# Kernel tuning notes

Measured on AMD Instinct MI355X. Metric: run time of the kernel, lower is better.

The kernel has to match this reference:

```python
import jax, jax.numpy as jnp
import numpy as np

HID, E, S, L_CAP, EPS = 768, 1536, 128, 512, 1e-5


def _rope_seq(x):
    """RoPE along axis 1. x: [b, n, 2, s]."""
    n, s = x.shape[1], x.shape[-1]
    half = s // 2
    inv_freq = jnp.power(10000.0, -jnp.arange(half, dtype=x.dtype) / half)  # [half]
    sinusoid = jnp.arange(n, dtype=x.dtype)[:, None, None] * inv_freq       # [n,1,half]
    sin, cos = jnp.sin(sinusoid), jnp.cos(sinusoid)
    x1, x2 = jnp.split(x, 2, axis=-1)
    return jnp.concatenate([x1 * cos - x2 * sin, x2 * cos + x1 * sin], axis=-1)


def setup_inputs() -> dict:
    key = jax.random.key(0)
    ks = jax.random.split(key, 6)
    B, L = 32, 512
    return {
        "x": jax.random.normal(ks[0], (B, L, HID), dtype=jnp.float32),
        "ln_gamma": jnp.ones((HID,), jnp.float32),
        "ln_beta": jnp.zeros((HID,), jnp.float32),
        "uv_W": jax.random.normal(ks[1], (HID, 2 * E + S), jnp.float32) * 0.02,
        "uv_b": jnp.zeros((2 * E + S,), jnp.float32),
        "gamma_qk": jax.random.normal(ks[2], (2, S), jnp.float32) * 0.02,
        "beta_qk": jnp.zeros((2, S), jnp.float32),
        "w_rel": jax.random.normal(ks[3], (2 * L_CAP - 1,), jnp.float32) * 0.02,
        "o_W": jax.random.normal(ks[4], (E, HID), jnp.float32) * 0.02,
        "o_b": jnp.zeros((HID,), jnp.float32),
    }


def reference(x, ln_gamma, ln_beta, uv_W, uv_b, gamma_qk, beta_qk, w_rel, o_W, o_b):
    L = x.shape[1]
    shortcut = x
    # LayerNorm
    mu = jnp.mean(x, axis=-1, keepdims=True)
    var = jnp.mean(jnp.square(x - mu), axis=-1, keepdims=True)
    xn = (x - mu) * jax.lax.rsqrt(var + EPS) * ln_gamma + ln_beta
    # uv projection + silu, split into u, v, base
    uv = jax.nn.silu(xn @ uv_W + uv_b)                       # [b, n, 2e+s]
    u, v, base = jnp.split(uv, [E, 2 * E], axis=-1)          # [b,n,e], [b,n,e], [b,n,s]
    # per-head affine then RoPE -> q, k
    base = base[..., None, :] * gamma_qk + beta_qk           # [b, n, 2, s]
    base = _rope_seq(base)
    q, k = base[..., 0, :], base[..., 1, :]
    # relu^2 attention kernel with Toeplitz relative position bias
    qk = jnp.einsum('bnd,bmd->bnm', q, k)
    idx = jnp.arange(L)
    bias = w_rel[idx[None, :] - idx[:, None] + L - 1]        # bias[i,j] = w[j-i+L-1]
    kernel = jnp.square(jax.nn.relu(qk / L + bias))
    # gated value aggregation + output projection + residual
    out = u * jnp.einsum('bnm,bme->bne', kernel, v)
    out = out @ o_W + o_b
    return out + shortcut
```

## Files before the change

kernel.cpp:

```cpp
#include <hip/hip_runtime.h>
#include <hip/hip_bf16.h>
#include <math.h>

typedef __bf16 bf16x8 __attribute__((ext_vector_type(8)));
typedef float f32x4 __attribute__((ext_vector_type(4)));
typedef unsigned short u16x4 __attribute__((ext_vector_type(4)));

#define AS1P const __attribute__((address_space(1))) void*
#define AS3P __attribute__((address_space(3))) void*

__device__ __forceinline__ float b2f(unsigned short h) {
    unsigned int u = ((unsigned int)h) << 16;
    return __builtin_bit_cast(float, u);
}
__device__ __forceinline__ unsigned short f2b(float f) {
    unsigned int u = __builtin_bit_cast(unsigned int, f);
    u += 0x7FFFu + ((u >> 16) & 1u);
    return (unsigned short)(u >> 16);
}
__device__ __forceinline__ float silu(float c) {
    return c * __builtin_amdgcn_rcpf(1.0f + __expf(-c));
}

__global__ __launch_bounds__(256) void k_convT(const float* __restrict__ src,
                                               unsigned short* __restrict__ dst,
                                               int R, int C) {
    __shared__ float tile[32][33];
    int tx = threadIdx.x, ty = threadIdx.y;
    int r0 = blockIdx.y << 5, c0 = blockIdx.x << 5;
#pragma unroll
    for (int i = 0; i < 4; ++i)
        tile[ty + 8 * i][tx] = src[(long long)(r0 + ty + 8 * i) * C + c0 + tx];
    __syncthreads();
#pragma unroll
    for (int i = 0; i < 4; ++i)
        dst[(long long)(c0 + ty + 8 * i) * R + r0 + tx] = f2b(tile[tx][ty + 8 * i]);
}

__global__ __launch_bounds__(256) void k_ln(const float* __restrict__ x,
                                            const float* __restrict__ g,
                                            const float* __restrict__ b,
                                            unsigned short* __restrict__ xn) {
    int row = blockIdx.x;
    int t = threadIdx.x;
    const float* xr = x + (long long)row * 768;
    float v0 = xr[t], v1 = xr[t + 256], v2 = xr[t + 512];
    float s = v0 + v1 + v2;
    float q = v0 * v0 + v1 * v1 + v2 * v2;
#pragma unroll
    for (int off = 32; off > 0; off >>= 1) {
        s += __shfl_xor(s, off);
        q += __shfl_xor(q, off);
    }
    __shared__ float ss[4], sq[4];
    int w = t >> 6;
    if ((t & 63) == 0) { ss[w] = s; sq[w] = q; }
    __syncthreads();
    float S_ = ss[0] + ss[1] + ss[2] + ss[3];
    float Q_ = sq[0] + sq[1] + sq[2] + sq[3];
    float mu = S_ * (1.0f / 768.0f);
    float var = Q_ * (1.0f / 768.0f) - mu * mu;
    float rs = rsqrtf(var + 1e-5f);
    unsigned short* xo = xn + (long long)row * 768;
    xo[t]       = f2b((v0 - mu) * rs * g[t]       + b[t]);
    xo[t + 256] = f2b((v1 - mu) * rs * g[t + 256] + b[t + 256]);
    xo[t + 512] = f2b((v2 - mu) * rs * g[t + 512] + b[t + 512]);
}

__global__ __launch_bounds__(128) void k_rope(const unsigned short* __restrict__ bS,
                                              const float* __restrict__ gqk,
                                              const float* __restrict__ bqk,
                                              unsigned short* __restrict__ q,
                                              unsigned short* __restrict__ k) {
    int row = blockIdx.x;
    int l = row & 511;
    int s = threadIdx.x;
    int j = s & 63;
    int partner = s ^ 64;
    float b0 = b2f(bS[(long long)row * 128 + s]);
    float bp = b2f(bS[(long long)row * 128 + partner]);
    float invf = __expf((float)j * -0.14391156831f);
    float th = (float)l * invf;
    float sn, cs;
    __sincosf(th, &sn, &cs);
    float sign = (s < 64) ? -1.0f : 1.0f;
    float preq  = b0 * gqk[s]           + bqk[s];
    float preqp = bp * gqk[partner]     + bqk[partner];
    q[(long long)row * 128 + s] = f2b(preq * cs + sign * preqp * sn);
    float prek  = b0 * gqk[128 + s]       + bqk[128 + s];
    float prekp = bp * gqk[128 + partner] + bqk[128 + partner];
    k[(long long)row * 128 + s] = f2b(prek * cs + sign * prekp * sn);
}

__global__ __launch_bounds__(256) void k_qk(const unsigned short* __restrict__ A,
                                            const unsigned short* __restrict__ B,
                                            const float* __restrict__ wrel,
                                            unsigned short* __restrict__ P) {
    __shared__ __align__(16) unsigned short As[128 * 64];
    __shared__ __align__(16) unsigned short Bs[128 * 64];
    int t = threadIdx.x;
    int w = t >> 6, lane = t & 63;
    int wr = w >> 1, wc = w & 1;
    int bx = blockIdx.x, by = blockIdx.y, bz = blockIdx.z;
    const unsigned short* Ab = A + (long long)bz * 512 * 128 + (long long)by * 128 * 128;
    const unsigned short* Bb = B + (long long)bz * 512 * 128 + (long long)bx * 128 * 128;

    f32x4 acc[4][4];
#pragma unroll
    for (int m = 0; m < 4; ++m)
#pragma unroll
        for (int n = 0; n < 4; ++n) acc[m][n] = (f32x4){0.f, 0.f, 0.f, 0.f};

    int rowA = (w << 3) + (lane >> 3);
    int colA = (lane & 7) << 3;

    for (int k0 = 0; k0 < 128; k0 += 64) {
#pragma unroll
        for (int i = 0; i < 4; ++i) {
            int r = (i << 5) + rowA;
            __builtin_amdgcn_global_load_lds(
                (AS1P)(Ab + (long long)r * 128 + k0 + colA),
                (AS3P)(&As[(i << 11) + (w << 9)]), 16, 0, 0);
            __builtin_amdgcn_global_load_lds(
                (AS1P)(Bb + (long long)r * 128 + k0 + colA),
                (AS3P)(&Bs[(i << 11) + (w << 9)]), 16, 0, 0);
        }
        __syncthreads();
#pragma unroll
        for (int ks = 0; ks < 2; ++ks) {
            bf16x8 af[4], bfr[4];
#pragma unroll
            for (int m = 0; m < 4; ++m)
                af[m] = *(const bf16x8*)&As[((wr << 6) + (m << 4) + (lane & 15)) * 64 +
                                            (ks << 5) + ((lane >> 4) << 3)];
#pragma unroll
            for (int n = 0; n < 4; ++n)
                bfr[n] = *(const bf16x8*)&Bs[((wc << 6) + (n << 4) + (lane & 15)) * 64 +
                                             (ks << 5) + ((lane >> 4) << 3)];
#pragma unroll
            for (int m = 0; m < 4; ++m)
#pragma unroll
                for (int n = 0; n < 4; ++n)
                    acc[m][n] = __builtin_amdgcn_mfma_f32_16x16x32_bf16(bfr[n], af[m],
                                                                        acc[m][n], 0, 0, 0);
        }
        __syncthreads();
    }

    int c15 = lane & 15, qq = lane >> 4;
    int rowb = (by << 7) + (wr << 6) + c15;
    int colb = (bx << 7) + (wc << 6) + (qq << 2);
#pragma unroll
    for (int m = 0; m < 4; ++m) {
#pragma unroll
        for (int n = 0; n < 4; ++n) {
            int grow = rowb + (m << 4);
            int gcol = colb + (n << 4);
            f32x4 a = acc[m][n];
            int base = gcol - grow + 511;
            u16x4 o;
#pragma unroll
            for (int i = 0; i < 4; ++i) {
                float val = a[i] * (1.0f / 512.0f) + wrel[base + i];
                val = fmaxf(val, 0.0f);
                o[i] = f2b(val * val);
            }
            *(u16x4*)(P + ((long long)(bz * 512 + grow)) * 512 + gcol) = o;
        }
    }
}

__device__ __forceinline__ bf16x8 ldsread(const unsigned short* p) {
    bf16x8 r;
    unsigned int off =
        (unsigned int)(unsigned long long)(__attribute__((address_space(3))) const void*)p;
    asm volatile("ds_read_b128 %0, %1" : "=v"(r) : "v"(off));
    return r;
}
__device__ __forceinline__ bf16x8 frag32(const unsigned short* tile, int r, int qq) {
    return ldsread(tile + r * 32 + ((qq ^ ((r >> 1) & 3)) << 3));
}
template <int ROWS, int K>
__device__ __forceinline__ void stage_t(const unsigned short* __restrict__ g,
                                        unsigned short* lds, int t) {
#pragma unroll
    for (int i = 0; i < ROWS / 64; ++i) {
        int slot = t + (i << 8);
        int row = slot >> 2;
        int gs = (slot & 3) ^ ((row >> 1) & 3);
        __builtin_amdgcn_global_load_lds(
            (AS1P)(g + (long long)row * K + (gs << 3)),
            (AS3P)(lds + slot * 8), 16, 0, 0);
    }
}

template <bool SWAP, int NT>
__device__ __forceinline__ void ring_kloop(const unsigned short* __restrict__ Ab,
                                           const unsigned short* __restrict__ Bb,
                                           unsigned short* As0, unsigned short* As1,
                                           unsigned short* Bs0, unsigned short* Bs1,
                                           f32x4 (&acc)[8][4], int t, int wc, int c15, int qq) {
    constexpr int K = NT * 32;
    stage_t<128, K>(Ab, As0, t);
    stage_t<256, K>(Bb, Bs0, t);
    stage_t<128, K>(Ab + 32, As1, t);
    stage_t<256, K>(Bb + 32, Bs1, t);
    for (int kt = 0; kt < NT; ++kt) {
        if (kt < NT - 1)
            asm volatile("s_waitcnt vmcnt(6)" ::: "memory");
        else
            asm volatile("s_waitcnt vmcnt(0)" ::: "memory");
        __builtin_amdgcn_s_barrier();
        __builtin_amdgcn_sched_barrier(0);
        const unsigned short* At = (kt & 1) ? As1 : As0;
        const unsigned short* Bt = (kt & 1) ? Bs1 : Bs0;
        bf16x8 af[8], bfr[4];
#pragma unroll
        for (int n = 0; n < 4; ++n) bfr[n] = frag32(Bt, wc * 64 + n * 16 + c15, qq);
#pragma unroll
        for (int m = 0; m < 8; ++m) af[m] = frag32(At, m * 16 + c15, qq);
        asm volatile("s_waitcnt lgkmcnt(0)" ::: "memory");
        __builtin_amdgcn_sched_barrier(0);
        __builtin_amdgcn_s_barrier();
        if (kt + 2 < NT) {
            unsigned short* Asn = (kt & 1) ? As1 : As0;
            unsigned short* Bsn = (kt & 1) ? Bs1 : Bs0;
            stage_t<128, K>(Ab + (long long)(kt + 2) * 32, Asn, t);
            stage_t<256, K>(Bb + (long long)(kt + 2) * 32, Bsn, t);
        }
        __builtin_amdgcn_s_setprio(1);
#pragma unroll
        for (int m = 0; m < 8; ++m)
#pragma unroll
            for (int n = 0; n < 4; ++n) {
                if constexpr (SWAP)
                    acc[m][n] = __builtin_amdgcn_mfma_f32_16x16x32_bf16(bfr[n], af[m],
                                                                        acc[m][n], 0, 0, 0);
                else
                    acc[m][n] = __builtin_amdgcn_mfma_f32_16x16x32_bf16(af[m], bfr[n],
                                                                        acc[m][n], 0, 0, 0);
            }
        __builtin_amdgcn_s_setprio(0);
    }
}

template <int EPI, bool SWZ, int NT>
__global__ __launch_bounds__(256, 2) void k_ring(const unsigned short* __restrict__ A,
                                                 const unsigned short* __restrict__ B,
                                                 long long strideA, long long strideB,
                                                 void* p0, void* p1, void* p2,
                                                 const void* p3) {
    constexpr int K = NT * 32;
    __shared__ __align__(16) unsigned short As[2][128 * 32];
    __shared__ __align__(16) unsigned short Bs[2][256 * 32];
    int t = threadIdx.x;
    int w = t >> 6, lane = t & 63;
    int wc = w, c15 = lane & 15, qq = lane >> 4;
    int bx = blockIdx.x, by = blockIdx.y, bz = blockIdx.z;
    if constexpr (SWZ) {
        int gx = gridDim.x;
        int nb = gx * gridDim.y;
        int bid = by * gx + bx;
        int s = (bid & 7) * (nb >> 3) + (bid >> 3);
        bx = s % gx;
        by = s / gx;
    }
    const unsigned short* Ab = A + bz * strideA + (long long)by * 128 * K;
    const unsigned short* Bb = B + bz * strideB + (long long)bx * 256 * K;

    f32x4 acc[8][4];
#pragma unroll
    for (int m = 0; m < 8; ++m)
#pragma unroll
        for (int n = 0; n < 4; ++n) acc[m][n] = (f32x4){0.f, 0.f, 0.f, 0.f};

    bool swapped = true;
    if constexpr (EPI == 10) {
        swapped = !(bx >= 6 && bx < 12);
        if (swapped)
            ring_kloop<true, NT>(Ab, Bb, &As[0][0], &As[1][0], &Bs[0][0], &Bs[1][0],
                                 acc, t, wc, c15, qq);
        else
            ring_kloop<false, NT>(Ab, Bb, &As[0][0], &As[1][0], &Bs[0][0], &Bs[1][0],
                                  acc, t, wc, c15, qq);
    } else {
        ring_kloop<true, NT>(Ab, Bb, &As[0][0], &As[1][0], &Bs[0][0], &Bs[1][0],
                             acc, t, wc, c15, qq);
    }

    if constexpr (EPI == 10) {
        if (swapped) {
            int rowb = by * 128 + c15;
            int colb = bx * 256 + wc * 64 + (qq << 2);
#pragma unroll
            for (int m = 0; m < 8; ++m) {
#pragma unroll
                for (int n = 0; n < 4; ++n) {
                    int R = rowb + m * 16;
                    int C = colb + n * 16;
                    f32x4 a = acc[m][n];
                    if (C < 1536) {
                        f32x4 bb = *(const f32x4*)((const float*)p3 + C);
                        u16x4 o;
#pragma unroll
                        for (int i = 0; i < 4; ++i) o[i] = f2b(silu(a[i] + bb[i]));
                        *(u16x4*)((unsigned short*)p0 + (long long)R * 1536 + C) = o;
                    } else if (C < 3200) {
                        f32x4 bb = *(const f32x4*)((const float*)p3 + C);
                        u16x4 o;
#pragma unroll
                        for (int i = 0; i < 4; ++i) o[i] = f2b(silu(a[i] + bb[i]));
                        *(u16x4*)((unsigned short*)p2 + (long long)R * 128 + (C - 3072)) = o;
                    }
                }
            }
        } else {
            int rowb = by * 128 + (qq << 2);
            int colb = bx * 256 + wc * 64 + c15;
#pragma unroll
            for (int m = 0; m < 8; ++m) {
#pragma unroll
                for (int n = 0; n < 4; ++n) {
                    int R = rowb + m * 16;
                    int C = colb + n * 16;
                    float bias = ((const float*)p3)[C];
                    f32x4 a = acc[m][n];
                    u16x4 o;
#pragma unroll
                    for (int i = 0; i < 4; ++i) o[i] = f2b(silu(a[i] + bias));
                    int bb2 = R >> 9, mm = R & 511;
                    *(u16x4*)((unsigned short*)p1 +
                              ((long long)bb2 * 1536 + (C - 1536)) * 512 + mm) = o;
                }
            }
        }
    } else if constexpr (EPI == 2) {
        int rowb = by * 128 + c15;
        int colb = bx * 256 + wc * 64 + (qq << 2);
#pragma unroll
        for (int m = 0; m < 8; ++m) {
#pragma unroll
            for (int n = 0; n < 4; ++n) {
                int R = rowb + m * 16;
                int C = colb + n * 16;
                f32x4 a = acc[m][n];
                long long idx = ((long long)(bz * 512 + R)) * 1536 + C;
                u16x4 uu = *(const u16x4*)((const unsigned short*)p1 + idx);
                u16x4 o;
#pragma unroll
                for (int i = 0; i < 4; ++i) o[i] = f2b(a[i] * b2f(uu[i]));
                *(u16x4*)((unsigned short*)p0 + idx) = o;
            }
        }
    } else {
        int rowb = by * 128 + c15;
        int colb = bx * 256 + wc * 64 + (qq << 2);
#pragma unroll
        for (int m = 0; m < 8; ++m) {
#pragma unroll
            for (int n = 0; n < 4; ++n) {
                int R = rowb + m * 16;
                int C = colb + n * 16;
                f32x4 a = acc[m][n];
                long long idx = (long long)R * 768 + C;
                f32x4 xv = *(const f32x4*)((const float*)p2 + idx);
                f32x4 ob = *(const f32x4*)((const float*)p1 + C);
                f32x4 o;
#pragma unroll
                for (int i = 0; i < 4; ++i) o[i] = a[i] + ob[i] + xv[i];
                *(f32x4*)((float*)p0 + idx) = o;
            }
        }
    }
}

extern "C" void kernel_launch(void* const* d_in, const int* in_sizes, int n_in,
                              void* d_out, int out_size, void* d_ws, size_t ws_size,
                              hipStream_t stream) {
    const float* x     = (const float*)d_in[0];
    const float* ln_g  = (const float*)d_in[1];
    const float* ln_b  = (const float*)d_in[2];
    const float* uv_W  = (const float*)d_in[3];
    const float* uv_b  = (const float*)d_in[4];
    const float* g_qk  = (const float*)d_in[5];
    const float* b_qk  = (const float*)d_in[6];
    const float* w_rel = (const float*)d_in[7];
    const float* o_W   = (const float*)d_in[8];
    const float* o_b   = (const float*)d_in[9];
    float* out = (float*)d_out;

    char* ws = (char*)d_ws;
    size_t off = 0;
    auto alloc = [&](size_t bytes) {
        void* p = ws + off;
        off += (bytes + 255) & ~(size_t)255;
        return p;
    };
    unsigned short* uvWT = (unsigned short*)alloc(3200ll * 768 * 2);
    unsigned short* oWT  = (unsigned short*)alloc(768ll * 1536 * 2);
    unsigned short* xn   = (unsigned short*)alloc(16384ll * 768 * 2);
    unsigned short* u    = (unsigned short*)alloc(16384ll * 1536 * 2);
    unsigned short* vT   = (unsigned short*)alloc(32ll * 1536 * 512 * 2);
    unsigned short* bS   = (unsigned short*)alloc(16384ll * 128 * 2);
    unsigned short* q    = (unsigned short*)alloc(32ll * 512 * 128 * 2);
    unsigned short* k    = (unsigned short*)alloc(32ll * 512 * 128 * 2);
    unsigned short* P     = xn;
    unsigned short* gated = u;

    k_convT<<<dim3(100, 24), dim3(32, 8), 0, stream>>>(uv_W, uvWT, 768, 3200);
    k_convT<<<dim3(24, 48), dim3(32, 8), 0, stream>>>(o_W, oWT, 1536, 768);
    k_ln<<<16384, 256, 0, stream>>>(x, ln_g, ln_b, xn);
    k_ring<10, true, 24><<<dim3(13, 128), 256, 0, stream>>>(
        xn, uvWT, 0, 0, (void*)u, (void*)vT, (void*)bS, (const void*)uv_b);
    k_rope<<<16384, 128, 0, stream>>>(bS, g_qk, b_qk, q, k);
    k_qk<<<dim3(4, 4, 32), 256, 0, stream>>>(q, k, w_rel, P);
    k_ring<2, false, 16><<<dim3(6, 4, 32), 256, 0, stream>>>(
        P, vT, 512ll * 512, 1536ll * 512, (void*)gated, (void*)u, nullptr, nullptr);
    k_ring<3, true, 48><<<dim3(3, 128), 256, 0, stream>>>(
        gated, oWT, 0, 0, (void*)out, (void*)o_b, (void*)x, nullptr);
}
```

Measured before the change: 300.5 us.

## Triple-buffer LDS ring in GEMM k-loop to drop second barrier

The shared-memory staging for the GEMM k-loop grows from two slots to a three-slot ring. The prefetch of tile kt+2 is now issued right after the top-of-iteration barrier, into the slot last read at kt-1. This removes the second barrier per k-step and lets global-to-LDS loads start earlier, overlapping them with the fragment reads and MFMAs. In exchange, LDS use per block rises from 48KB to 72KB, which could limit occupancy under the two-blocks-per-CU launch bound.

```diff
diff --git a/kernel.cpp b/kernel.cpp
--- a/kernel.cpp
+++ b/kernel.cpp
@@ -197,14 +197,15 @@
 template <bool SWAP, int NT>
 __device__ __forceinline__ void ring_kloop(const unsigned short* __restrict__ Ab,
                                            const unsigned short* __restrict__ Bb,
-                                           unsigned short* As0, unsigned short* As1,
-                                           unsigned short* Bs0, unsigned short* Bs1,
+                                           unsigned short* As, unsigned short* Bs,
                                            f32x4 (&acc)[8][4], int t, int wc, int c15, int qq) {
     constexpr int K = NT * 32;
-    stage_t<128, K>(Ab, As0, t);
-    stage_t<256, K>(Bb, Bs0, t);
-    stage_t<128, K>(Ab + 32, As1, t);
-    stage_t<256, K>(Bb + 32, Bs1, t);
+    constexpr int ASLOT = 128 * 32, BSLOT = 256 * 32;
+    stage_t<128, K>(Ab, As, t);
+    stage_t<256, K>(Bb, Bs, t);
+    stage_t<128, K>(Ab + 32, As + ASLOT, t);
+    stage_t<256, K>(Bb + 32, Bs + BSLOT, t);
+    int slot = 0;
     for (int kt = 0; kt < NT; ++kt) {
         if (kt < NT - 1)
             asm volatile("s_waitcnt vmcnt(6)" ::: "memory");
@@ -212,8 +213,14 @@
             asm volatile("s_waitcnt vmcnt(0)" ::: "memory");
         __builtin_amdgcn_s_barrier();
         __builtin_amdgcn_sched_barrier(0);
-        const unsigned short* At = (kt & 1) ? As1 : As0;
-        const unsigned short* Bt = (kt & 1) ? Bs1 : Bs0;
+        if (kt + 2 < NT) {
+            int ns = slot + 2;
+            if (ns >= 3) ns -= 3;
+            stage_t<128, K>(Ab + (long long)(kt + 2) * 32, As + ns * ASLOT, t);
+            stage_t<256, K>(Bb + (long long)(kt + 2) * 32, Bs + ns * BSLOT, t);
+        }
+        const unsigned short* At = As + slot * ASLOT;
+        const unsigned short* Bt = Bs + slot * BSLOT;
         bf16x8 af[8], bfr[4];
 #pragma unroll
         for (int n = 0; n < 4; ++n) bfr[n] = frag32(Bt, wc * 64 + n * 16 + c15, qq);
@@ -221,13 +228,6 @@
         for (int m = 0; m < 8; ++m) af[m] = frag32(At, m * 16 + c15, qq);
         asm volatile("s_waitcnt lgkmcnt(0)" ::: "memory");
         __builtin_amdgcn_sched_barrier(0);
-        __builtin_amdgcn_s_barrier();
-        if (kt + 2 < NT) {
-            unsigned short* Asn = (kt & 1) ? As1 : As0;
-            unsigned short* Bsn = (kt & 1) ? Bs1 : Bs0;
-            stage_t<128, K>(Ab + (long long)(kt + 2) * 32, Asn, t);
-            stage_t<256, K>(Bb + (long long)(kt + 2) * 32, Bsn, t);
-        }
         __builtin_amdgcn_s_setprio(1);
 #pragma unroll
         for (int m = 0; m < 8; ++m)
@@ -241,6 +241,7 @@
                                                                         acc[m][n], 0, 0, 0);
             }
         __builtin_amdgcn_s_setprio(0);
+        slot = (slot + 1 == 3) ? 0 : slot + 1;
     }
 }
 
@@ -251,8 +252,8 @@
                                                  void* p0, void* p1, void* p2,
                                                  const void* p3) {
     constexpr int K = NT * 32;
-    __shared__ __align__(16) unsigned short As[2][128 * 32];
-    __shared__ __align__(16) unsigned short Bs[2][256 * 32];
+    __shared__ __align__(16) unsigned short As[3][128 * 32];
+    __shared__ __align__(16) unsigned short Bs[3][256 * 32];
     int t = threadIdx.x;
     int w = t >> 6, lane = t & 63;
     int wc = w, c15 = lane & 15, qq = lane >> 4;
@@ -278,14 +279,11 @@
     if constexpr (EPI == 10) {
         swapped = !(bx >= 6 && bx < 12);
         if (swapped)
-            ring_kloop<true, NT>(Ab, Bb, &As[0][0], &As[1][0], &Bs[0][0], &Bs[1][0],
-                                 acc, t, wc, c15, qq);
+            ring_kloop<true, NT>(Ab, Bb, &As[0][0], &Bs[0][0], acc, t, wc, c15, qq);
         else
-            ring_kloop<false, NT>(Ab, Bb, &As[0][0], &As[1][0], &Bs[0][0], &Bs[1][0],
-                                  acc, t, wc, c15, qq);
+            ring_kloop<false, NT>(Ab, Bb, &As[0][0], &Bs[0][0], acc, t, wc, c15, qq);
     } else {
-        ring_kloop<true, NT>(Ab, Bb, &As[0][0], &As[1][0], &Bs[0][0], &Bs[1][0],
-                             acc, t, wc, c15, qq);
+        ring_kloop<true, NT>(Ab, Bb, &As[0][0], &Bs[0][0], acc, t, wc, c15, qq);
     }
 
     if constexpr (EPI == 10) {
```

Result: no change. 296.7 us (-1.3%).
